# Performance work log

Hardware: AMD Instinct MI355X
Metric: run time of the kernel (lower is better)

Reference implementation:

```python
import jax, jax.numpy as jnp
import numpy as np

P = 7              # output_size (7,7)
SCALE = 0.125      # spatial_scale
B, C, H, W = 4, 256, 128, 128
K = 512
IMG = H / SCALE    # 1024 px image space


def setup_inputs() -> dict:
    key = jax.random.key(0)
    k1, k2, k3, k4 = jax.random.split(key, 4)
    inputs = jax.random.normal(k1, (B, C, H, W), dtype=jnp.float32)
    # rois: [K,5] = (batch_idx, x1, y1, x2, y2) in image coordinates
    bidx = jax.random.randint(k2, (K, 1), 0, B).astype(jnp.float32)
    xy = jax.random.uniform(k3, (K, 4), minval=0.0, maxval=IMG, dtype=jnp.float32)
    x1 = jnp.minimum(xy[:, 0], xy[:, 2])
    x2 = jnp.clip(jnp.maximum(xy[:, 0], xy[:, 2]), x1 + 8.0, IMG)
    y1 = jnp.minimum(xy[:, 1], xy[:, 3])
    y2 = jnp.clip(jnp.maximum(xy[:, 1], xy[:, 3]), y1 + 8.0, IMG)
    rois = jnp.stack([bidx[:, 0], x1, y1, x2, y2], axis=1)
    # per-ROI binary spatial mask over the feature map (pixel used iff > 0.5)
    masks = (jax.random.uniform(k4, (K, H, W)) > 0.2).astype(jnp.float32)
    return {"inputs": inputs, "rois": rois, "masks": masks}


def reference(inputs, rois, masks):
    Hh, Ww = inputs.shape[2], inputs.shape[3]
    hr = jnp.arange(Hh)
    wr = jnp.arange(Ww)
    pr = jnp.arange(P)
    neg = -jnp.inf

    def pool_one(args):
        roi, mask = args
        b = roi[0].astype(jnp.int32)
        f = jax.lax.dynamic_index_in_dim(inputs, b, 0, keepdims=False)  # [C,H,W]
        # torchvision-style rounded ROI bounds in feature-map coords
        sw = jnp.round(roi[1] * SCALE).astype(jnp.int32)
        sh = jnp.round(roi[2] * SCALE).astype(jnp.int32)
        ew = jnp.round(roi[3] * SCALE).astype(jnp.int32)
        eh = jnp.round(roi[4] * SCALE).astype(jnp.int32)
        roi_w = jnp.maximum(ew - sw + 1, 1)
        roi_h = jnp.maximum(eh - sh + 1, 1)
        # per-output-bin [start,end) row/col ranges (floor/ceil adaptive bins)
        hs = jnp.clip((pr * roi_h) // P + sh, 0, Hh)
        he = jnp.clip(((pr + 1) * roi_h + P - 1) // P + sh, 0, Hh)
        ws = jnp.clip((pr * roi_w) // P + sw, 0, Ww)
        we = jnp.clip(((pr + 1) * roi_w + P - 1) // P + sw, 0, Ww)
        rowmask = (hr[None, :] >= hs[:, None]) & (hr[None, :] < he[:, None])  # [P,H]
        colmask = (wr[None, :] >= ws[:, None]) & (wr[None, :] < we[:, None])  # [P,W]
        fm = jnp.where(mask > 0.5, f, neg)                                   # [C,H,W]
        # separable max: rows first, then cols (bins are rectangles)
        m1 = jnp.max(jnp.where(rowmask[:, None, :, None], fm[None], neg), axis=2)      # [P,C,W]
        m2 = jnp.max(jnp.where(colmask[None, :, None, :], m1[:, None], neg), axis=3)   # [Ph,Pw,C]
        out = jnp.where(jnp.isinf(m2), 0.0, m2)  # empty / fully-masked bin -> 0
        return jnp.transpose(out, (2, 0, 1))     # [C,P,P]

    return jax.lax.map(pool_one, (rois, masks))  # [K,C,P,P]
```

## Files before the change

### kernel.cpp

```cpp
#include <hip/hip_runtime.h>
#include <math.h>

#define P 7
#define SCALE 0.125f
#define BB 4
#define CC 256
#define HH 128
#define WW 128
#define KK 512
#define NBIN 49
#define GPB 13
#define NXCD 8
#define RPX  (KK / NXCD)

#define TRANS_BLOCKS 4096
#define MASK_BLOCKS  4096

__device__ __forceinline__ unsigned short f32_to_bf16_rne(float f) {
    unsigned int u = __float_as_uint(f);
    u += 0x7FFFu + ((u >> 16) & 1u);
    return (unsigned short)(u >> 16);
}

__device__ __forceinline__ unsigned short bf16_key(unsigned short b) {
    return (b & 0x8000u) ? (unsigned short)(~b) : (unsigned short)(b | 0x8000u);
}

__device__ __forceinline__ unsigned int pkmax_u16(unsigned int a, unsigned int b) {
    unsigned int d;
    asm("v_pk_max_u16 %0, %1, %2" : "=v"(d) : "v"(a), "v"(b));
    return d;
}

__global__ __launch_bounds__(1024) void prep_fused(
    const float* __restrict__ in, const float* __restrict__ masks,
    const float* __restrict__ rois,
    unsigned short* __restrict__ out, unsigned long long* __restrict__ mbits,
    int* __restrict__ perm)
{
    __shared__ float tile[64][65];
    __shared__ int skey[KK];
    const int bid = blockIdx.x;
    const int tid = threadIdx.x;

    if (bid < TRANS_BLOCKS) {
        const int p0 = (bid & 255) * 64;
        const int c0 = ((bid >> 8) & 3) * 64;
        const int b  = bid >> 10;
        const int tx = tid & 63;
        const int ty = tid >> 6;

        const float* src = in + (size_t)b * CC * (HH * WW);
#pragma unroll
        for (int j = 0; j < 64; j += 16)
            tile[ty + j][tx] =
                __builtin_nontemporal_load(&src[(size_t)(c0 + ty + j) * (HH * WW) + p0 + tx]);
        __syncthreads();

        unsigned int* dst = (unsigned int*)(out + (size_t)b * (HH * WW) * CC);
#pragma unroll
        for (int i = 0; i < 2; ++i) {
            const int flat = i * 1024 + tid;
            const int px = flat >> 5;
            const int cp = flat & 31;
            const unsigned int lo = bf16_key(f32_to_bf16_rne(tile[cp * 2][px]));
            const unsigned int hi = bf16_key(f32_to_bf16_rne(tile[cp * 2 + 1][px]));
            dst[((size_t)(p0 + px) * CC + c0) / 2 + cp] = lo | (hi << 16);
        }

        if (bid == 0) {
            __syncthreads();
            if (tid < KK) {
                const float* r = rois + (size_t)tid * 5;
                const int rb = (int)r[0];
                int rsh = (int)rintf(r[2] * SCALE);
                rsh = min(max(rsh, 0), HH - 1);
                skey[tid] = rb * HH + rsh;
            }
            __syncthreads();
            if (tid < KK) {
                const int mykey = skey[tid];
                int pos = 0;
                for (int j = 0; j < KK; ++j) {
                    const int kj = skey[j];
                    pos += (kj < mykey) || (kj == mykey && j < tid);
                }
                perm[pos] = tid;
            }
        }
    } else {
        const int mbid = bid - TRANS_BLOCKS;
        const int wv   = tid >> 6;
        const int lane = tid & 63;
        const int row  = mbid * 16 + wv;
        const float* mr = masks + (size_t)row * WW;
        const unsigned long long b0 = __ballot(mr[lane] > 0.5f);
        const unsigned long long b1 = __ballot(mr[64 + lane] > 0.5f);
        if (lane == 0) {
            mbits[(size_t)row * 2]     = b0;
            mbits[(size_t)row * 2 + 1] = b1;
        }
    }
}

__global__ __launch_bounds__(256) void pool_key(
    const unsigned int* __restrict__ fbase,
    const float* __restrict__ rois,
    const unsigned long long* __restrict__ mbits,
    const int* __restrict__ perm,
    float* __restrict__ out)
{
    const int pid = blockIdx.x;
    const int x   = pid & (NXCD - 1);
    const int t   = pid >> 3;
    const int g   = t % GPB;
    const int q   = t / GPB;
    const int k   = __builtin_amdgcn_readfirstlane(perm[x * RPX + q]);

    const int wv   = threadIdx.x >> 6;
    const int lane = threadIdx.x & 63;
    const int bi   = g * 4 + wv;
    if (bi >= NBIN) return;
    const int ph = bi / P;
    const int pw = bi % P;

    const int half = lane >> 5;
    const int c4   = (lane & 31) * 4;

    const float* roi = rois + (size_t)k * 5;
    const int b  = __builtin_amdgcn_readfirstlane((int)roi[0]);
    const int sw = (int)rintf(roi[1] * SCALE);
    const int sh = (int)rintf(roi[2] * SCALE);
    const int ew = (int)rintf(roi[3] * SCALE);
    const int eh = (int)rintf(roi[4] * SCALE);
    const int roi_w = max(ew - sw + 1, 1);
    const int roi_h = max(eh - sh + 1, 1);

    const int hs = __builtin_amdgcn_readfirstlane(min(max((ph * roi_h) / P + sh, 0), HH));
    const int he = __builtin_amdgcn_readfirstlane(min(max(((ph + 1) * roi_h + P - 1) / P + sh, 0), HH));
    const int wl = __builtin_amdgcn_readfirstlane(min(max((pw * roi_w) / P + sw, 0), WW));
    const int wr = __builtin_amdgcn_readfirstlane(min(max(((pw + 1) * roi_w + P - 1) / P + sw, 0), WW));

    const unsigned int* fb = fbase
        + (unsigned int)b * (unsigned int)(HH * WW * (CC / 2))
        + (unsigned int)(half * (CC / 2) + c4);
    const unsigned long long* mrow = mbits + (size_t)k * (HH * 2);

    unsigned int a0 = 0, a1 = 0, a2 = 0, a3 = 0;

    const int sh0 = 0 + half, sh1 = 2 + half, sh2 = 4 + half, sh3 = 6 + half;

#pragma unroll 4
    for (int h = hs; h < he; ++h) {
        const unsigned long long lov = mrow[2 * h];
        const unsigned long long hiv = mrow[2 * h + 1];
        const unsigned int ll  = __builtin_amdgcn_readfirstlane((unsigned int)lov);
        const unsigned int lh  = __builtin_amdgcn_readfirstlane((unsigned int)(lov >> 32));
        const unsigned int hl  = __builtin_amdgcn_readfirstlane((unsigned int)hiv);
        const unsigned int hh2 = __builtin_amdgcn_readfirstlane((unsigned int)(hiv >> 32));
        const unsigned long long lo = ((unsigned long long)lh << 32) | ll;
        const unsigned long long hi = ((unsigned long long)hh2 << 32) | hl;

        const unsigned int* frow = fb + (unsigned int)h * (unsigned int)(WW * (CC / 2));
        for (int w0 = wl; w0 < wr; w0 += 8) {
            unsigned long long v;
            if (w0 >= 64)      v = hi >> (w0 - 64);
            else if (w0 == 0)  v = lo;
            else               v = (lo >> w0) | (hi << (64 - w0));
            unsigned int chunk = (unsigned int)v & 0xFFu;
            const int n = wr - w0;
            chunk &= (n >= 8) ? 0xFFu : ((1u << n) - 1u);

            const unsigned int* basep = frow + (unsigned int)w0 * (CC / 2);
            const uint4 k0 = *(const uint4*)(basep);
            const uint4 k1 = *(const uint4*)(basep + 256);
            const uint4 k2 = *(const uint4*)(basep + 512);
            const uint4 k3 = *(const uint4*)(basep + 768);

            const unsigned int m0 = 0u - ((chunk >> sh0) & 1u);
            const unsigned int m1 = 0u - ((chunk >> sh1) & 1u);
            const unsigned int m2 = 0u - ((chunk >> sh2) & 1u);
            const unsigned int m3 = 0u - ((chunk >> sh3) & 1u);

            a0 = pkmax_u16(a0, k0.x & m0); a1 = pkmax_u16(a1, k0.y & m0);
            a2 = pkmax_u16(a2, k0.z & m0); a3 = pkmax_u16(a3, k0.w & m0);
            a0 = pkmax_u16(a0, k1.x & m1); a1 = pkmax_u16(a1, k1.y & m1);
            a2 = pkmax_u16(a2, k1.z & m1); a3 = pkmax_u16(a3, k1.w & m1);
            a0 = pkmax_u16(a0, k2.x & m2); a1 = pkmax_u16(a1, k2.y & m2);
            a2 = pkmax_u16(a2, k2.z & m2); a3 = pkmax_u16(a3, k2.w & m2);
            a0 = pkmax_u16(a0, k3.x & m3); a1 = pkmax_u16(a1, k3.y & m3);
            a2 = pkmax_u16(a2, k3.z & m3); a3 = pkmax_u16(a3, k3.w & m3);
        }
    }

    a0 = pkmax_u16(a0, (unsigned int)__shfl_xor((int)a0, 32, 64));
    a1 = pkmax_u16(a1, (unsigned int)__shfl_xor((int)a1, 32, 64));
    a2 = pkmax_u16(a2, (unsigned int)__shfl_xor((int)a2, 32, 64));
    a3 = pkmax_u16(a3, (unsigned int)__shfl_xor((int)a3, 32, 64));

    if (half == 0) {
        const unsigned int acc[4] = {a0, a1, a2, a3};
        float* o = out + ((size_t)k * CC + (size_t)c4 * 2) * NBIN + ph * P + pw;
#pragma unroll
        for (int j = 0; j < 8; ++j) {
            const unsigned int d = acc[j >> 1];
            const unsigned int key = (j & 1) ? (d >> 16) : (d & 0xFFFFu);
            float r;
            if (key == 0u) {
                r = 0.0f;
            } else {
                const unsigned int bbits =
                    (key & 0x8000u) ? (key ^ 0x8000u) : (~key & 0xFFFFu);
                r = __uint_as_float(bbits << 16);
            }
            o[(size_t)j * NBIN] = r;
        }
    }
}

__global__ __launch_bounds__(256) void ROIPool_nchw_kernel(
    const float* __restrict__ inputs, const float* __restrict__ rois,
    const float* __restrict__ masks, float* __restrict__ out)
{
    const int k  = blockIdx.x;
    const int ph = blockIdx.y;
    const int c  = threadIdx.x;

    const float* roi = rois + k * 5;
    const int b  = (int)roi[0];
    const int sw = (int)rintf(roi[1] * SCALE);
    const int sh = (int)rintf(roi[2] * SCALE);
    const int ew = (int)rintf(roi[3] * SCALE);
    const int eh = (int)rintf(roi[4] * SCALE);
    const int roi_w = max(ew - sw + 1, 1);
    const int roi_h = max(eh - sh + 1, 1);

    const int hs = min(max((ph * roi_h) / P + sh, 0), HH);
    const int he = min(max(((ph + 1) * roi_h + P - 1) / P + sh, 0), HH);

    int wsb[P], web[P];
#pragma unroll
    for (int pw = 0; pw < P; ++pw) {
        wsb[pw] = min(max((pw * roi_w) / P + sw, 0), WW);
        web[pw] = min(max(((pw + 1) * roi_w + P - 1) / P + sw, 0), WW);
    }

    const float* f = inputs + ((size_t)b * CC + c) * (HH * WW);
    const float* m = masks  + (size_t)k * (HH * WW);

    float vmax[P];
#pragma unroll
    for (int pw = 0; pw < P; ++pw) vmax[pw] = -INFINITY;

    for (int h = hs; h < he; ++h) {
        const float* frow = f + h * WW;
        const float* mrow = m + h * WW;
#pragma unroll
        for (int pw = 0; pw < P; ++pw) {
            float v = vmax[pw];
            for (int w = wsb[pw]; w < web[pw]; ++w)
                if (mrow[w] > 0.5f) v = fmaxf(v, frow[w]);
            vmax[pw] = v;
        }
    }

    float* o = out + (((size_t)k * CC + c) * P + ph) * P;
#pragma unroll
    for (int pw = 0; pw < P; ++pw) {
        const float v = vmax[pw];
        o[pw] = isinf(v) ? 0.0f : v;
    }
}

extern "C" void kernel_launch(void* const* d_in, const int* in_sizes, int n_in,
                              void* d_out, int out_size, void* d_ws, size_t ws_size,
                              hipStream_t stream) {
    const float* inputs = (const float*)d_in[0];
    const float* rois   = (const float*)d_in[1];
    const float* masks  = (const float*)d_in[2];
    float* out = (float*)d_out;

    const size_t keys_bytes  = (size_t)BB * CC * HH * WW * sizeof(unsigned short);
    const size_t mbits_bytes = (size_t)KK * HH * 2 * sizeof(unsigned long long);
    const size_t perm_bytes  = (size_t)KK * sizeof(int);

    if (ws_size >= keys_bytes + mbits_bytes + perm_bytes) {
        unsigned short* fT = (unsigned short*)d_ws;
        unsigned long long* mb = (unsigned long long*)((char*)d_ws + keys_bytes);
        int* perm = (int*)((char*)d_ws + keys_bytes + mbits_bytes);
        {
            dim3 grid(TRANS_BLOCKS + MASK_BLOCKS);
            dim3 block(1024);
            prep_fused<<<grid, block, 0, stream>>>(inputs, masks, rois, fT, mb, perm);
        }
        {
            dim3 grid(KK * GPB);
            dim3 block(256);
            pool_key<<<grid, block, 0, stream>>>((const unsigned int*)fT, rois, mb, perm, out);
        }
    } else {
        dim3 grid(KK, P);
        dim3 block(CC);
        ROIPool_nchw_kernel<<<grid, block, 0, stream>>>(inputs, rois, masks, out);
    }
}
```

Measured before the change: 114.0 us.

## Pool a full row strip of seven bins per wavefront instead of one bin

The pooling kernel now assigns each wavefront an entire output row (ph) and loops over all seven column bins, keeping seven accumulator sets in registers. The grid shrinks from 13 blocks per ROI to 2, so the per-row mask-bit loads and ROI setup are shared across bins and the seven output writes per channel become contiguous. In exchange there is much less parallelism (1024 blocks with up to 4 waves each), more registers per thread, and a longer serial loop per wave, which may leave the GPU underoccupied.

```diff
diff --git a/kernel.cpp b/kernel.cpp
--- a/kernel.cpp
+++ b/kernel.cpp
@@ -9,7 +9,6 @@
 #define WW 128
 #define KK 512
 #define NBIN 49
-#define GPB 13
 #define NXCD 8
 #define RPX  (KK / NXCD)
 
@@ -103,7 +102,7 @@
     }
 }
 
-__global__ __launch_bounds__(256) void pool_key(
+__global__ __launch_bounds__(256) void pool_strip(
     const unsigned int* __restrict__ fbase,
     const float* __restrict__ rois,
     const unsigned long long* __restrict__ mbits,
@@ -113,16 +112,14 @@
     const int pid = blockIdx.x;
     const int x   = pid & (NXCD - 1);
     const int t   = pid >> 3;
-    const int g   = t % GPB;
-    const int q   = t / GPB;
+    const int q   = t >> 1;
+    const int s   = t & 1;
     const int k   = __builtin_amdgcn_readfirstlane(perm[x * RPX + q]);
 
     const int wv   = threadIdx.x >> 6;
     const int lane = threadIdx.x & 63;
-    const int bi   = g * 4 + wv;
-    if (bi >= NBIN) return;
-    const int ph = bi / P;
-    const int pw = bi % P;
+    const int ph   = s * 4 + wv;
+    if (ph >= P) return;
 
     const int half = lane >> 5;
     const int c4   = (lane & 31) * 4;
@@ -138,19 +135,27 @@
 
     const int hs = __builtin_amdgcn_readfirstlane(min(max((ph * roi_h) / P + sh, 0), HH));
     const int he = __builtin_amdgcn_readfirstlane(min(max(((ph + 1) * roi_h + P - 1) / P + sh, 0), HH));
-    const int wl = __builtin_amdgcn_readfirstlane(min(max((pw * roi_w) / P + sw, 0), WW));
-    const int wr = __builtin_amdgcn_readfirstlane(min(max(((pw + 1) * roi_w + P - 1) / P + sw, 0), WW));
+
+    int wsb[P], web[P];
+#pragma unroll
+    for (int j = 0; j < P; ++j) {
+        wsb[j] = __builtin_amdgcn_readfirstlane(min(max((j * roi_w) / P + sw, 0), WW));
+        web[j] = __builtin_amdgcn_readfirstlane(min(max(((j + 1) * roi_w + P - 1) / P + sw, 0), WW));
+    }
 
     const unsigned int* fb = fbase
         + (unsigned int)b * (unsigned int)(HH * WW * (CC / 2))
         + (unsigned int)(half * (CC / 2) + c4);
     const unsigned long long* mrow = mbits + (size_t)k * (HH * 2);
 
-    unsigned int a0 = 0, a1 = 0, a2 = 0, a3 = 0;
+    unsigned int acc[P][4];
+#pragma unroll
+    for (int j = 0; j < P; ++j) {
+        acc[j][0] = 0; acc[j][1] = 0; acc[j][2] = 0; acc[j][3] = 0;
+    }
 
     const int sh0 = 0 + half, sh1 = 2 + half, sh2 = 4 + half, sh3 = 6 + half;
 
-#pragma unroll 4
     for (int h = hs; h < he; ++h) {
         const unsigned long long lov = mrow[2 * h];
         const unsigned long long hiv = mrow[2 * h + 1];
@@ -162,58 +167,76 @@
         const unsigned long long hi = ((unsigned long long)hh2 << 32) | hl;
 
         const unsigned int* frow = fb + (unsigned int)h * (unsigned int)(WW * (CC / 2));
-        for (int w0 = wl; w0 < wr; w0 += 8) {
-            unsigned long long v;
-            if (w0 >= 64)      v = hi >> (w0 - 64);
-            else if (w0 == 0)  v = lo;
-            else               v = (lo >> w0) | (hi << (64 - w0));
-            unsigned int chunk = (unsigned int)v & 0xFFu;
-            const int n = wr - w0;
-            chunk &= (n >= 8) ? 0xFFu : ((1u << n) - 1u);
-
-            const unsigned int* basep = frow + (unsigned int)w0 * (CC / 2);
-            const uint4 k0 = *(const uint4*)(basep);
-            const uint4 k1 = *(const uint4*)(basep + 256);
-            const uint4 k2 = *(const uint4*)(basep + 512);
-            const uint4 k3 = *(const uint4*)(basep + 768);
-
-            const unsigned int m0 = 0u - ((chunk >> sh0) & 1u);
-            const unsigned int m1 = 0u - ((chunk >> sh1) & 1u);
-            const unsigned int m2 = 0u - ((chunk >> sh2) & 1u);
-            const unsigned int m3 = 0u - ((chunk >> sh3) & 1u);
-
-            a0 = pkmax_u16(a0, k0.x & m0); a1 = pkmax_u16(a1, k0.y & m0);
-            a2 = pkmax_u16(a2, k0.z & m0); a3 = pkmax_u16(a3, k0.w & m0);
-            a0 = pkmax_u16(a0, k1.x & m1); a1 = pkmax_u16(a1, k1.y & m1);
-            a2 = pkmax_u16(a2, k1.z & m1); a3 = pkmax_u16(a3, k1.w & m1);
-            a0 = pkmax_u16(a0, k2.x & m2); a1 = pkmax_u16(a1, k2.y & m2);
-            a2 = pkmax_u16(a2, k2.z & m2); a3 = pkmax_u16(a3, k2.w & m2);
-            a0 = pkmax_u16(a0, k3.x & m3); a1 = pkmax_u16(a1, k3.y & m3);
-            a2 = pkmax_u16(a2, k3.z & m3); a3 = pkmax_u16(a3, k3.w & m3);
-        }
-    }
-
-    a0 = pkmax_u16(a0, (unsigned int)__shfl_xor((int)a0, 32, 64));
-    a1 = pkmax_u16(a1, (unsigned int)__shfl_xor((int)a1, 32, 64));
-    a2 = pkmax_u16(a2, (unsigned int)__shfl_xor((int)a2, 32, 64));
-    a3 = pkmax_u16(a3, (unsigned int)__shfl_xor((int)a3, 32, 64));
+
+#pragma unroll
+        for (int j = 0; j < P; ++j) {
+            const int bl = wsb[j], br = web[j];
+            for (int w0 = bl; w0 < br; w0 += 8) {
+                unsigned long long v;
+                if (w0 >= 64)      v = hi >> (w0 - 64);
+                else if (w0 == 0)  v = lo;
+                else               v = (lo >> w0) | (hi << (64 - w0));
+                unsigned int chunk = (unsigned int)v & 0xFFu;
+                const int n = br - w0;
+                chunk &= (n >= 8) ? 0xFFu : ((1u << n) - 1u);
+
+                const unsigned int* basep = frow + (unsigned int)w0 * (CC / 2);
+                const uint4 k0 = *(const uint4*)(basep);
+                const uint4 k1 = *(const uint4*)(basep + 256);
+                const uint4 k2 = *(const uint4*)(basep + 512);
+                const uint4 k3 = *(const uint4*)(basep + 768);
+
+                const unsigned int m0 = 0u - ((chunk >> sh0) & 1u);
+                const unsigned int m1 = 0u - ((chunk >> sh1) & 1u);
+                const unsigned int m2 = 0u - ((chunk >> sh2) & 1u);
+                const unsigned int m3 = 0u - ((chunk >> sh3) & 1u);
+
+                acc[j][0] = pkmax_u16(acc[j][0], k0.x & m0);
+                acc[j][1] = pkmax_u16(acc[j][1], k0.y & m0);
+                acc[j][2] = pkmax_u16(acc[j][2], k0.z & m0);
+                acc[j][3] = pkmax_u16(acc[j][3], k0.w & m0);
+                acc[j][0] = pkmax_u16(acc[j][0], k1.x & m1);
+                acc[j][1] = pkmax_u16(acc[j][1], k1.y & m1);
+                acc[j][2] = pkmax_u16(acc[j][2], k1.z & m1);
+                acc[j][3] = pkmax_u16(acc[j][3], k1.w & m1);
+                acc[j][0] = pkmax_u16(acc[j][0], k2.x & m2);
+                acc[j][1] = pkmax_u16(acc[j][1], k2.y & m2);
+                acc[j][2] = pkmax_u16(acc[j][2], k2.z & m2);
+                acc[j][3] = pkmax_u16(acc[j][3], k2.w & m2);
+                acc[j][0] = pkmax_u16(acc[j][0], k3.x & m3);
+                acc[j][1] = pkmax_u16(acc[j][1], k3.y & m3);
+                acc[j][2] = pkmax_u16(acc[j][2], k3.z & m3);
+                acc[j][3] = pkmax_u16(acc[j][3], k3.w & m3);
+            }
+        }
+    }
+
+#pragma unroll
+    for (int j = 0; j < P; ++j) {
+        acc[j][0] = pkmax_u16(acc[j][0], (unsigned int)__shfl_xor((int)acc[j][0], 32, 64));
+        acc[j][1] = pkmax_u16(acc[j][1], (unsigned int)__shfl_xor((int)acc[j][1], 32, 64));
+        acc[j][2] = pkmax_u16(acc[j][2], (unsigned int)__shfl_xor((int)acc[j][2], 32, 64));
+        acc[j][3] = pkmax_u16(acc[j][3], (unsigned int)__shfl_xor((int)acc[j][3], 32, 64));
+    }
 
     if (half == 0) {
-        const unsigned int acc[4] = {a0, a1, a2, a3};
-        float* o = out + ((size_t)k * CC + (size_t)c4 * 2) * NBIN + ph * P + pw;
+        float* o = out + ((size_t)k * CC + (size_t)c4 * 2) * NBIN + ph * P;
 #pragma unroll
         for (int j = 0; j < 8; ++j) {
-            const unsigned int d = acc[j >> 1];
-            const unsigned int key = (j & 1) ? (d >> 16) : (d & 0xFFFFu);
-            float r;
-            if (key == 0u) {
-                r = 0.0f;
-            } else {
-                const unsigned int bbits =
-                    (key & 0x8000u) ? (key ^ 0x8000u) : (~key & 0xFFFFu);
-                r = __uint_as_float(bbits << 16);
+#pragma unroll
+            for (int pwv = 0; pwv < P; ++pwv) {
+                const unsigned int d = acc[pwv][j >> 1];
+                const unsigned int key = (j & 1) ? (d >> 16) : (d & 0xFFFFu);
+                float r;
+                if (key == 0u) {
+                    r = 0.0f;
+                } else {
+                    const unsigned int bbits =
+                        (key & 0x8000u) ? (key ^ 0x8000u) : (~key & 0xFFFFu);
+                    r = __uint_as_float(bbits << 16);
+                }
+                o[(size_t)j * NBIN + pwv] = r;
             }
-            o[(size_t)j * NBIN] = r;
         }
     }
 }
@@ -294,9 +317,9 @@
             prep_fused<<<grid, block, 0, stream>>>(inputs, masks, rois, fT, mb, perm);
         }
         {
-            dim3 grid(KK * GPB);
+            dim3 grid(KK * 2);
             dim3 block(256);
-            pool_key<<<grid, block, 0, stream>>>((const unsigned int*)fT, rois, mb, perm, out);
+            pool_strip<<<grid, block, 0, stream>>>((const unsigned int*)fT, rois, mb, perm, out);
         }
     } else {
         dim3 grid(KK, P);
```

New measurement: 162.3 us. 42.4% more time.

## Pair adjacent column bins per wave and precompute ROI bin bounds in prep

Applied to the files above, without the earlier changes.

Each wave now handles two horizontally adjacent output bins in the same row band, so the mask-row loads and loop overhead are shared and the grid shrinks from 13 to 7 blocks per ROI. The prep kernel now computes packed per-ROI row/column bin bounds and a sorted (roi,batch) table, replacing the per-block ROI arithmetic and the perm lookup. In exchange, the fourth pair in each row carries a dummy seventh bin, so some wave work is idle. Register pressure also rises from the second accumulator set, and the mask words are no longer forced scalar with readfirstlane.

```diff
diff --git a/kernel.cpp b/kernel.cpp
--- a/kernel.cpp
+++ b/kernel.cpp
@@ -9,7 +9,6 @@
 #define WW 128
 #define KK 512
 #define NBIN 49
-#define GPB 13
 #define NXCD 8
 #define RPX  (KK / NXCD)
 
@@ -36,7 +35,8 @@
     const float* __restrict__ in, const float* __restrict__ masks,
     const float* __restrict__ rois,
     unsigned short* __restrict__ out, unsigned long long* __restrict__ mbits,
-    int* __restrict__ perm)
+    unsigned int* __restrict__ kb, unsigned short* __restrict__ rowb,
+    unsigned short* __restrict__ colb)
 {
     __shared__ float tile[64][65];
     __shared__ int skey[KK];
@@ -85,7 +85,26 @@
                     const int kj = skey[j];
                     pos += (kj < mykey) || (kj == mykey && j < tid);
                 }
-                perm[pos] = tid;
+                const float* r = rois + (size_t)tid * 5;
+                const int b  = (int)r[0];
+                const int sw = (int)rintf(r[1] * SCALE);
+                const int sh = (int)rintf(r[2] * SCALE);
+                const int ew = (int)rintf(r[3] * SCALE);
+                const int eh = (int)rintf(r[4] * SCALE);
+                const int roi_w = max(ew - sw + 1, 1);
+                const int roi_h = max(eh - sh + 1, 1);
+                kb[pos] = (unsigned int)tid | ((unsigned int)b << 16);
+#pragma unroll
+                for (int j = 0; j < P; ++j) {
+                    const int hs = min(max((j * roi_h) / P + sh, 0), HH);
+                    const int he = min(max(((j + 1) * roi_h + P - 1) / P + sh, 0), HH);
+                    const int ws = min(max((j * roi_w) / P + sw, 0), WW);
+                    const int we = min(max(((j + 1) * roi_w + P - 1) / P + sw, 0), WW);
+                    rowb[(pos << 3) + j] = (unsigned short)(hs | (he << 8));
+                    colb[(pos << 3) + j] = (unsigned short)(ws | (we << 8));
+                }
+                rowb[(pos << 3) + 7] = 0;
+                colb[(pos << 3) + 7] = 0;
             }
         }
     } else {
@@ -103,117 +122,128 @@
     }
 }
 
-__global__ __launch_bounds__(256) void pool_key(
+__global__ __launch_bounds__(256) void pool_pair(
     const unsigned int* __restrict__ fbase,
-    const float* __restrict__ rois,
+    const unsigned int* __restrict__ kb,
+    const unsigned short* __restrict__ rowb,
+    const unsigned short* __restrict__ colb,
     const unsigned long long* __restrict__ mbits,
-    const int* __restrict__ perm,
     float* __restrict__ out)
 {
     const int pid = blockIdx.x;
     const int x   = pid & (NXCD - 1);
     const int t   = pid >> 3;
-    const int g   = t % GPB;
-    const int q   = t / GPB;
-    const int k   = __builtin_amdgcn_readfirstlane(perm[x * RPX + q]);
+    const int g   = t % 7;
+    const int q   = t / 7;
+    const int i   = x * RPX + q;
 
     const int wv   = threadIdx.x >> 6;
     const int lane = threadIdx.x & 63;
-    const int bi   = g * 4 + wv;
-    if (bi >= NBIN) return;
-    const int ph = bi / P;
-    const int pw = bi % P;
+    const int u    = g * 4 + wv;
+    const int ph   = u >> 2;
+    const int bp   = u & 3;
+    const int j0   = bp * 2;
+    const int j1   = j0 + 1;
 
     const int half = lane >> 5;
     const int c4   = (lane & 31) * 4;
 
-    const float* roi = rois + (size_t)k * 5;
-    const int b  = __builtin_amdgcn_readfirstlane((int)roi[0]);
-    const int sw = (int)rintf(roi[1] * SCALE);
-    const int sh = (int)rintf(roi[2] * SCALE);
-    const int ew = (int)rintf(roi[3] * SCALE);
-    const int eh = (int)rintf(roi[4] * SCALE);
-    const int roi_w = max(ew - sw + 1, 1);
-    const int roi_h = max(eh - sh + 1, 1);
-
-    const int hs = __builtin_amdgcn_readfirstlane(min(max((ph * roi_h) / P + sh, 0), HH));
-    const int he = __builtin_amdgcn_readfirstlane(min(max(((ph + 1) * roi_h + P - 1) / P + sh, 0), HH));
-    const int wl = __builtin_amdgcn_readfirstlane(min(max((pw * roi_w) / P + sw, 0), WW));
-    const int wr = __builtin_amdgcn_readfirstlane(min(max(((pw + 1) * roi_w + P - 1) / P + sw, 0), WW));
+    const unsigned int kbv = kb[i];
+    const int k = kbv & 0xFFFF;
+    const int b = (kbv >> 16) & 0xFF;
+    const unsigned int rb  = rowb[(i << 3) + ph];
+    const unsigned int cb0 = colb[(i << 3) + j0];
+    const unsigned int cb1 = colb[(i << 3) + j1];
+    const int hs = rb & 0xFF,  he  = (rb >> 8) & 0xFF;
+    const int ws0 = cb0 & 0xFF, we0 = (cb0 >> 8) & 0xFF;
+    const int ws1 = cb1 & 0xFF, we1 = (cb1 >> 8) & 0xFF;
 
     const unsigned int* fb = fbase
         + (unsigned int)b * (unsigned int)(HH * WW * (CC / 2))
         + (unsigned int)(half * (CC / 2) + c4);
     const unsigned long long* mrow = mbits + (size_t)k * (HH * 2);
 
-    unsigned int a0 = 0, a1 = 0, a2 = 0, a3 = 0;
+    unsigned int p0 = 0, p1 = 0, p2 = 0, p3 = 0;
+    unsigned int r0 = 0, r1 = 0, r2 = 0, r3 = 0;
 
     const int sh0 = 0 + half, sh1 = 2 + half, sh2 = 4 + half, sh3 = 6 + half;
 
-#pragma unroll 4
+#define DO_BIN(BL, BR, A0, A1, A2, A3) do {                                    \
+        for (int w0 = (BL); w0 < (BR); w0 += 8) {                              \
+            unsigned long long v;                                              \
+            if (w0 >= 64)      v = hi >> (w0 - 64);                            \
+            else if (w0 == 0)  v = lo;                                         \
+            else               v = (lo >> w0) | (hi << (64 - w0));             \
+            unsigned int chunk = (unsigned int)v & 0xFFu;                      \
+            const int n = (BR) - w0;                                           \
+            chunk &= (n >= 8) ? 0xFFu : ((1u << n) - 1u);                      \
+            const unsigned int* basep = frow + (unsigned int)w0 * (CC / 2);    \
+            const uint4 k0 = *(const uint4*)(basep);                           \
+            const uint4 k1 = *(const uint4*)(basep + 256);                     \
+            const uint4 k2 = *(const uint4*)(basep + 512);                     \
+            const uint4 k3 = *(const uint4*)(basep + 768);                     \
+            const unsigned int m0 = 0u - ((chunk >> sh0) & 1u);                \
+            const unsigned int m1 = 0u - ((chunk >> sh1) & 1u);                \
+            const unsigned int m2 = 0u - ((chunk >> sh2) & 1u);                \
+            const unsigned int m3 = 0u - ((chunk >> sh3) & 1u);                \
+            A0 = pkmax_u16(A0, k0.x & m0); A1 = pkmax_u16(A1, k0.y & m0);      \
+            A2 = pkmax_u16(A2, k0.z & m0); A3 = pkmax_u16(A3, k0.w & m0);      \
+            A0 = pkmax_u16(A0, k1.x & m1); A1 = pkmax_u16(A1, k1.y & m1);      \
+            A2 = pkmax_u16(A2, k1.z & m1); A3 = pkmax_u16(A3, k1.w & m1);      \
+            A0 = pkmax_u16(A0, k2.x & m2); A1 = pkmax_u16(A1, k2.y & m2);      \
+            A2 = pkmax_u16(A2, k2.z & m2); A3 = pkmax_u16(A3, k2.w & m2);      \
+            A0 = pkmax_u16(A0, k3.x & m3); A1 = pkmax_u16(A1, k3.y & m3);      \
+            A2 = pkmax_u16(A2, k3.z & m3); A3 = pkmax_u16(A3, k3.w & m3);      \
+        }                                                                      \
+    } while (0)
+
+#pragma unroll 2
     for (int h = hs; h < he; ++h) {
-        const unsigned long long lov = mrow[2 * h];
-        const unsigned long long hiv = mrow[2 * h + 1];
-        const unsigned int ll  = __builtin_amdgcn_readfirstlane((unsigned int)lov);
-        const unsigned int lh  = __builtin_amdgcn_readfirstlane((unsigned int)(lov >> 32));
-        const unsigned int hl  = __builtin_amdgcn_readfirstlane((unsigned int)hiv);
-        const unsigned int hh2 = __builtin_amdgcn_readfirstlane((unsigned int)(hiv >> 32));
-        const unsigned long long lo = ((unsigned long long)lh << 32) | ll;
-        const unsigned long long hi = ((unsigned long long)hh2 << 32) | hl;
-
+        const unsigned long long lo = mrow[2 * h];
+        const unsigned long long hi = mrow[2 * h + 1];
         const unsigned int* frow = fb + (unsigned int)h * (unsigned int)(WW * (CC / 2));
-        for (int w0 = wl; w0 < wr; w0 += 8) {
-            unsigned long long v;
-            if (w0 >= 64)      v = hi >> (w0 - 64);
-            else if (w0 == 0)  v = lo;
-            else               v = (lo >> w0) | (hi << (64 - w0));
-            unsigned int chunk = (unsigned int)v & 0xFFu;
-            const int n = wr - w0;
-            chunk &= (n >= 8) ? 0xFFu : ((1u << n) - 1u);
-
-            const unsigned int* basep = frow + (unsigned int)w0 * (CC / 2);
-            const uint4 k0 = *(const uint4*)(basep);
-            const uint4 k1 = *(const uint4*)(basep + 256);
-            const uint4 k2 = *(const uint4*)(basep + 512);
-            const uint4 k3 = *(const uint4*)(basep + 768);
-
-            const unsigned int m0 = 0u - ((chunk >> sh0) & 1u);
-            const unsigned int m1 = 0u - ((chunk >> sh1) & 1u);
-            const unsigned int m2 = 0u - ((chunk >> sh2) & 1u);
-            const unsigned int m3 = 0u - ((chunk >> sh3) & 1u);
-
-            a0 = pkmax_u16(a0, k0.x & m0); a1 = pkmax_u16(a1, k0.y & m0);
-            a2 = pkmax_u16(a2, k0.z & m0); a3 = pkmax_u16(a3, k0.w & m0);
-            a0 = pkmax_u16(a0, k1.x & m1); a1 = pkmax_u16(a1, k1.y & m1);
-            a2 = pkmax_u16(a2, k1.z & m1); a3 = pkmax_u16(a3, k1.w & m1);
-            a0 = pkmax_u16(a0, k2.x & m2); a1 = pkmax_u16(a1, k2.y & m2);
-            a2 = pkmax_u16(a2, k2.z & m2); a3 = pkmax_u16(a3, k2.w & m2);
-            a0 = pkmax_u16(a0, k3.x & m3); a1 = pkmax_u16(a1, k3.y & m3);
-            a2 = pkmax_u16(a2, k3.z & m3); a3 = pkmax_u16(a3, k3.w & m3);
-        }
-    }
-
-    a0 = pkmax_u16(a0, (unsigned int)__shfl_xor((int)a0, 32, 64));
-    a1 = pkmax_u16(a1, (unsigned int)__shfl_xor((int)a1, 32, 64));
-    a2 = pkmax_u16(a2, (unsigned int)__shfl_xor((int)a2, 32, 64));
-    a3 = pkmax_u16(a3, (unsigned int)__shfl_xor((int)a3, 32, 64));
+        DO_BIN(ws0, we0, p0, p1, p2, p3);
+        DO_BIN(ws1, we1, r0, r1, r2, r3);
+    }
+#undef DO_BIN
+
+    p0 = pkmax_u16(p0, (unsigned int)__shfl_xor((int)p0, 32, 64));
+    p1 = pkmax_u16(p1, (unsigned int)__shfl_xor((int)p1, 32, 64));
+    p2 = pkmax_u16(p2, (unsigned int)__shfl_xor((int)p2, 32, 64));
+    p3 = pkmax_u16(p3, (unsigned int)__shfl_xor((int)p3, 32, 64));
+    r0 = pkmax_u16(r0, (unsigned int)__shfl_xor((int)r0, 32, 64));
+    r1 = pkmax_u16(r1, (unsigned int)__shfl_xor((int)r1, 32, 64));
+    r2 = pkmax_u16(r2, (unsigned int)__shfl_xor((int)r2, 32, 64));
+    r3 = pkmax_u16(r3, (unsigned int)__shfl_xor((int)r3, 32, 64));
 
     if (half == 0) {
-        const unsigned int acc[4] = {a0, a1, a2, a3};
-        float* o = out + ((size_t)k * CC + (size_t)c4 * 2) * NBIN + ph * P + pw;
+        const unsigned int accA[4] = {p0, p1, p2, p3};
+        const unsigned int accB[4] = {r0, r1, r2, r3};
+        float* o = out + ((size_t)k * CC + (size_t)c4 * 2) * NBIN + ph * P;
 #pragma unroll
         for (int j = 0; j < 8; ++j) {
-            const unsigned int d = acc[j >> 1];
-            const unsigned int key = (j & 1) ? (d >> 16) : (d & 0xFFFFu);
-            float r;
-            if (key == 0u) {
-                r = 0.0f;
-            } else {
-                const unsigned int bbits =
-                    (key & 0x8000u) ? (key ^ 0x8000u) : (~key & 0xFFFFu);
-                r = __uint_as_float(bbits << 16);
+            const unsigned int dA = accA[j >> 1];
+            const unsigned int keyA = (j & 1) ? (dA >> 16) : (dA & 0xFFFFu);
+            float rA;
+            if (keyA == 0u) rA = 0.0f;
+            else {
+                const unsigned int bb =
+                    (keyA & 0x8000u) ? (keyA ^ 0x8000u) : (~keyA & 0xFFFFu);
+                rA = __uint_as_float(bb << 16);
             }
-            o[(size_t)j * NBIN] = r;
+            o[(size_t)j * NBIN + j0] = rA;
+            if (j1 < P) {
+                const unsigned int dB = accB[j >> 1];
+                const unsigned int keyB = (j & 1) ? (dB >> 16) : (dB & 0xFFFFu);
+                float rB;
+                if (keyB == 0u) rB = 0.0f;
+                else {
+                    const unsigned int bb =
+                        (keyB & 0x8000u) ? (keyB ^ 0x8000u) : (~keyB & 0xFFFFu);
+                    rB = __uint_as_float(bb << 16);
+                }
+                o[(size_t)j * NBIN + j1] = rB;
+            }
         }
     }
 }
@@ -282,21 +312,28 @@
 
     const size_t keys_bytes  = (size_t)BB * CC * HH * WW * sizeof(unsigned short);
     const size_t mbits_bytes = (size_t)KK * HH * 2 * sizeof(unsigned long long);
-    const size_t perm_bytes  = (size_t)KK * sizeof(int);
-
-    if (ws_size >= keys_bytes + mbits_bytes + perm_bytes) {
-        unsigned short* fT = (unsigned short*)d_ws;
-        unsigned long long* mb = (unsigned long long*)((char*)d_ws + keys_bytes);
-        int* perm = (int*)((char*)d_ws + keys_bytes + mbits_bytes);
+    const size_t kb_bytes    = (size_t)KK * sizeof(unsigned int);
+    const size_t rb_bytes    = (size_t)KK * 8 * sizeof(unsigned short);
+    const size_t cb_bytes    = (size_t)KK * 8 * sizeof(unsigned short);
+
+    if (ws_size >= keys_bytes + mbits_bytes + kb_bytes + rb_bytes + cb_bytes) {
+        char* p = (char*)d_ws;
+        unsigned short* fT = (unsigned short*)p;              p += keys_bytes;
+        unsigned long long* mb = (unsigned long long*)p;      p += mbits_bytes;
+        unsigned int* kb = (unsigned int*)p;                  p += kb_bytes;
+        unsigned short* rowb = (unsigned short*)p;            p += rb_bytes;
+        unsigned short* colb = (unsigned short*)p;
         {
             dim3 grid(TRANS_BLOCKS + MASK_BLOCKS);
             dim3 block(1024);
-            prep_fused<<<grid, block, 0, stream>>>(inputs, masks, rois, fT, mb, perm);
+            prep_fused<<<grid, block, 0, stream>>>(inputs, masks, rois, fT, mb,
+                                                   kb, rowb, colb);
         }
         {
-            dim3 grid(KK * GPB);
+            dim3 grid(KK * 7);
             dim3 block(256);
-            pool_key<<<grid, block, 0, stream>>>((const unsigned int*)fT, rois, mb, perm, out);
+            pool_pair<<<grid, block, 0, stream>>>((const unsigned int*)fT, kb,
+                                                  rowb, colb, mb, out);
         }
     } else {
         dim3 grid(KK, P);
```

Result: slower. 128.8 us (+13.1%).
